# Kernel tuning notes

Measured on AMD Instinct MI355X. Metric: run time of the kernel, lower is better.

## Reference

```python
import jax, jax.numpy as jnp
import numpy as np

N_OBJ = 1280
N_REL = 32768
HID = 512
POOL = 4096
N_OBJ_CLS = 151
N_REL_CLS = 51


def setup_inputs() -> dict:
    key = jax.random.key(0)
    ks = jax.random.split(key, 11)
    s = lambda d: 1.0 / np.sqrt(d)
    return {
        "edge_ctx": jax.random.normal(ks[0], (N_OBJ, HID), jnp.float32),
        "union_features": jax.random.normal(ks[1], (N_REL, POOL), jnp.float32),
        "w_post_emb": jax.random.normal(ks[2], (HID, 2 * HID), jnp.float32) * (10.0 * s(HID)),
        "b_post_emb": jax.random.normal(ks[3], (2 * HID,), jnp.float32) * 0.01,
        "w_post_cat": jax.random.normal(ks[4], (2 * HID, POOL), jnp.float32) * s(2 * HID),
        "b_post_cat": jnp.zeros((POOL,), jnp.float32),
        "w_ctx": jax.random.normal(ks[5], (POOL, N_REL_CLS), jnp.float32) * s(POOL),
        "b_ctx": jnp.zeros((N_REL_CLS,), jnp.float32),
        "freq_table": jax.random.normal(ks[6], (N_OBJ_CLS * N_OBJ_CLS, N_REL_CLS), jnp.float32),
        "obj_preds": jax.random.randint(ks[7], (N_OBJ,), 0, N_OBJ_CLS, jnp.int64),
        "pair_idx": jax.random.randint(ks[8], (N_REL, 2), 0, N_OBJ, jnp.int64),
    }


def reference(edge_ctx, union_features, w_post_emb, b_post_emb, w_post_cat,
              b_post_cat, w_ctx, b_ctx, freq_table, obj_preds, pair_idx):
    # edge_rep = relu(post_emb(edge_ctx)) viewed as [N_obj, 2, HID]
    edge_rep = jax.nn.relu(edge_ctx @ w_post_emb + b_post_emb)  # [N_obj, 2*HID]
    head_rep = edge_rep[:, :HID]   # [N_obj, HID]
    tail_rep = edge_rep[:, HID:]   # [N_obj, HID]
    # gather per-pair head/tail reps (pair_idx already globalized across images)
    prod_rep = jnp.concatenate(
        (head_rep[pair_idx[:, 0]], tail_rep[pair_idx[:, 1]]), axis=-1)  # [N_rel, 2*HID]
    prod_rep = prod_rep @ w_post_cat + b_post_cat                      # [N_rel, POOL]
    # elementwise fuse with visual union features, then compress to rel logits
    ctx_dists = (prod_rep * union_features) @ w_ctx + b_ctx            # [N_rel, 51]
    # frequency-bias embedding lookup on (subj_class, obj_class) pair
    pair_pred = jnp.stack((obj_preds[pair_idx[:, 0]], obj_preds[pair_idx[:, 1]]), axis=1)
    frq_dists = freq_table[pair_pred[:, 0] * N_OBJ_CLS + pair_pred[:, 1]]
    rel_dists = ctx_dists + frq_dists
    return rel_dists
```

## Files before the change

### kernel.cpp

```cpp
#include <hip/hip_runtime.h>

typedef __attribute__((ext_vector_type(8))) short bf16x8;
typedef __attribute__((ext_vector_type(4))) float f32x4;

__device__ __forceinline__ float bf2f(short s) {
    union { unsigned int i; float f; } v;
    v.i = ((unsigned int)(unsigned short)s) << 16;
    return v.f;
}
__device__ __forceinline__ short f2bf(float f) {
    unsigned int x = __float_as_uint(f);
    unsigned int r = (x + 0x7fffu + ((x >> 16) & 1u)) >> 16;
    return (short)r;
}

__global__ __launch_bounds__(256) void transpose_cvt(
    const float* __restrict__ in, short* __restrict__ out,
    int R, int C, int Cout)
{
    __shared__ short tile[64][65];
    const int r0 = blockIdx.x << 6;
    const int c0 = blockIdx.y << 6;
    const int t = threadIdx.x;
#pragma unroll
    for (int i = 0; i < 16; ++i) {
        int idx = t + (i << 8);
        int rr = idx >> 6, cc = idx & 63;
        int c = c0 + cc;
        tile[rr][cc] = (c < C) ? f2bf(in[(size_t)(r0 + rr) * C + c]) : (short)0;
    }
    __syncthreads();
#pragma unroll
    for (int i = 0; i < 16; ++i) {
        int idx = t + (i << 8);
        int cc = idx >> 6, rr = idx & 63;
        out[(size_t)(c0 + cc) * R + r0 + rr] = tile[rr][cc];
    }
}

template<int A_F32>
__global__ __launch_bounds__(256) void gemm_bt(
    const void* __restrict__ Ap, int lda,
    const short* __restrict__ Bt, int ldb,
    const float* __restrict__ bias,
    short* __restrict__ C, int ldc,
    int K, int relu)
{
    __shared__ short As[64][72];
    __shared__ short Bs[64][72];
    const int t = threadIdx.x;
    const int wave = t >> 6;
    const int lane = t & 63;
    const int m0 = blockIdx.x << 6;
    const int n0 = blockIdx.y << 6;

    const int rr = t >> 2;
    const int kc = (t & 3) << 4;
    const float* apf = (const float*)Ap + (size_t)(m0 + rr) * lda + kc;
    const short* aps = (const short*)Ap + (size_t)(m0 + rr) * lda + kc;
    const short* bp  = Bt + (size_t)(n0 + rr) * ldb + kc;

    f32x4 acc[4];
#pragma unroll
    for (int i = 0; i < 4; ++i) acc[i] = (f32x4){0.f, 0.f, 0.f, 0.f};

    const int ml = lane & 15;
    const int kq = (lane >> 4) << 3;

    for (int k0 = 0; k0 < K; k0 += 64) {
        bf16x8 a0, a1;
        if (A_F32) {
            float4 x0 = *(const float4*)(apf + k0);
            float4 x1 = *(const float4*)(apf + k0 + 4);
            float4 x2 = *(const float4*)(apf + k0 + 8);
            float4 x3 = *(const float4*)(apf + k0 + 12);
            a0[0] = f2bf(x0.x); a0[1] = f2bf(x0.y); a0[2] = f2bf(x0.z); a0[3] = f2bf(x0.w);
            a0[4] = f2bf(x1.x); a0[5] = f2bf(x1.y); a0[6] = f2bf(x1.z); a0[7] = f2bf(x1.w);
            a1[0] = f2bf(x2.x); a1[1] = f2bf(x2.y); a1[2] = f2bf(x2.z); a1[3] = f2bf(x2.w);
            a1[4] = f2bf(x3.x); a1[5] = f2bf(x3.y); a1[6] = f2bf(x3.z); a1[7] = f2bf(x3.w);
        } else {
            a0 = *(const bf16x8*)(aps + k0);
            a1 = *(const bf16x8*)(aps + k0 + 8);
        }
        bf16x8 b0 = *(const bf16x8*)(bp + k0);
        bf16x8 b1 = *(const bf16x8*)(bp + k0 + 8);
        __syncthreads();
        *(bf16x8*)&As[rr][kc]     = a0;
        *(bf16x8*)&As[rr][kc + 8] = a1;
        *(bf16x8*)&Bs[rr][kc]     = b0;
        *(bf16x8*)&Bs[rr][kc + 8] = b1;
        __syncthreads();
#pragma unroll
        for (int ks = 0; ks < 64; ks += 32) {
            bf16x8 af = *(const bf16x8*)&As[(wave << 4) + ml][ks + kq];
#pragma unroll
            for (int nb = 0; nb < 4; ++nb) {
                bf16x8 bfr = *(const bf16x8*)&Bs[(nb << 4) + ml][ks + kq];
                acc[nb] = __builtin_amdgcn_mfma_f32_16x16x32_bf16(af, bfr, acc[nb], 0, 0, 0);
            }
        }
    }

    const int ql = lane >> 4;
#pragma unroll
    for (int reg = 0; reg < 4; ++reg) {
        int r = m0 + (wave << 4) + (ql << 2) + reg;
#pragma unroll
        for (int nb = 0; nb < 4; ++nb) {
            int c = n0 + (nb << 4) + ml;
            float v = acc[nb][reg];
            if (bias) v += bias[c];
            if (relu) v = fmaxf(v, 0.f);
            C[(size_t)r * ldc + c] = f2bf(v);
        }
    }
}

__global__ __launch_bounds__(256) void fused_rel(
    const float* __restrict__ U,
    const short* __restrict__ Hm,
    const short* __restrict__ Tm,
    const short* __restrict__ Wt,
    const float* __restrict__ bcat,
    const float* __restrict__ bctx,
    const float* __restrict__ freq,
    const int* __restrict__ obj_preds,
    const int* __restrict__ pair_idx,
    float* __restrict__ out)
{
    __shared__ short As[64][72];
    __shared__ short Bs[64][72];
    const int t = threadIdx.x;
    const int wave = t >> 6;
    const int lane = t & 63;
    const int r0 = blockIdx.x << 6;

    const int rr = t >> 2;
    const int kc = (t & 3) << 4;

    const int r = r0 + rr;
    const int p0 = pair_idx[2 * r];
    const int p1 = pair_idx[2 * r + 1];

    const float* up = U + (size_t)r * 4096 + kc;
    const short* hp = Hm + (size_t)p0 * 4096 + kc;
    const short* tp = Tm + (size_t)p1 * 4096 + kc;
    const short* wp = Wt + (size_t)rr * 4096 + kc;
    const float* bp = bcat + kc;

    f32x4 acc[4];
#pragma unroll
    for (int i = 0; i < 4; ++i) acc[i] = (f32x4){0.f, 0.f, 0.f, 0.f};

    const int ml = lane & 15;
    const int kq = (lane >> 4) << 3;

    for (int k0 = 0; k0 < 4096; k0 += 64) {
        float4 u0 = *(const float4*)(up + k0);
        float4 u1 = *(const float4*)(up + k0 + 4);
        float4 u2 = *(const float4*)(up + k0 + 8);
        float4 u3 = *(const float4*)(up + k0 + 12);
        float4 c0 = *(const float4*)(bp + k0);
        float4 c1 = *(const float4*)(bp + k0 + 4);
        float4 c2 = *(const float4*)(bp + k0 + 8);
        float4 c3 = *(const float4*)(bp + k0 + 12);
        bf16x8 h0 = *(const bf16x8*)(hp + k0);
        bf16x8 h1 = *(const bf16x8*)(hp + k0 + 8);
        bf16x8 t0 = *(const bf16x8*)(tp + k0);
        bf16x8 t1 = *(const bf16x8*)(tp + k0 + 8);
        bf16x8 w0 = *(const bf16x8*)(wp + k0);
        bf16x8 w1 = *(const bf16x8*)(wp + k0 + 8);

        float uu[16] = {u0.x,u0.y,u0.z,u0.w, u1.x,u1.y,u1.z,u1.w,
                        u2.x,u2.y,u2.z,u2.w, u3.x,u3.y,u3.z,u3.w};
        float bb[16] = {c0.x,c0.y,c0.z,c0.w, c1.x,c1.y,c1.z,c1.w,
                        c2.x,c2.y,c2.z,c2.w, c3.x,c3.y,c3.z,c3.w};

        bf16x8 a0, a1;
#pragma unroll
        for (int j = 0; j < 8; ++j) {
            a0[j] = f2bf((bf2f(h0[j]) + bf2f(t0[j]) + bb[j])     * uu[j]);
            a1[j] = f2bf((bf2f(h1[j]) + bf2f(t1[j]) + bb[8 + j]) * uu[8 + j]);
        }
        __syncthreads();
        *(bf16x8*)&As[rr][kc]     = a0;
        *(bf16x8*)&As[rr][kc + 8] = a1;
        *(bf16x8*)&Bs[rr][kc]     = w0;
        *(bf16x8*)&Bs[rr][kc + 8] = w1;
        __syncthreads();
#pragma unroll
        for (int ks = 0; ks < 64; ks += 32) {
            bf16x8 af = *(const bf16x8*)&As[(wave << 4) + ml][ks + kq];
#pragma unroll
            for (int nb = 0; nb < 4; ++nb) {
                bf16x8 bfr = *(const bf16x8*)&Bs[(nb << 4) + ml][ks + kq];
                acc[nb] = __builtin_amdgcn_mfma_f32_16x16x32_bf16(af, bfr, acc[nb], 0, 0, 0);
            }
        }
    }

    const int ql = lane >> 4;
#pragma unroll
    for (int reg = 0; reg < 4; ++reg) {
        int rm = r0 + (wave << 4) + (ql << 2) + reg;
        int q0 = pair_idx[2 * rm];
        int q1 = pair_idx[2 * rm + 1];
        int code = obj_preds[q0] * 151 + obj_preds[q1];
        const float* fr = freq + (size_t)code * 51;
#pragma unroll
        for (int nb = 0; nb < 4; ++nb) {
            int c = (nb << 4) + ml;
            if (c < 51) {
                out[(size_t)rm * 51 + c] = acc[nb][reg] + bctx[c] + fr[c];
            }
        }
    }
}

extern "C" void kernel_launch(void* const* d_in, const int* in_sizes, int n_in,
                              void* d_out, int out_size, void* d_ws, size_t ws_size,
                              hipStream_t stream)
{
    (void)in_sizes; (void)n_in; (void)out_size; (void)ws_size;

    const float* edge_ctx = (const float*)d_in[0];
    const float* unionf   = (const float*)d_in[1];
    const float* w_emb    = (const float*)d_in[2];
    const float* b_emb    = (const float*)d_in[3];
    const float* w_cat    = (const float*)d_in[4];
    const float* b_cat    = (const float*)d_in[5];
    const float* w_ctx    = (const float*)d_in[6];
    const float* b_ctx    = (const float*)d_in[7];
    const float* freq     = (const float*)d_in[8];
    const int*   obj_pred = (const int*)d_in[9];
    const int*   pair_idx = (const int*)d_in[10];
    float* out = (float*)d_out;

    char* ws = (char*)d_ws;
    short* WembT    = (short*)(ws);
    short* WcatT    = (short*)(ws + (1ull  << 20));
    short* Wt       = (short*)(ws + (9ull  << 20));
    short* edge_rep = (short*)(ws + (10ull << 20));
    short* Hbuf     = (short*)(ws + (13ull << 20));
    short* Tbuf     = (short*)(ws + (23ull << 20));

    transpose_cvt<<<dim3(8, 16),  256, 0, stream>>>(w_emb, WembT, 512, 1024, 1024);
    transpose_cvt<<<dim3(16, 64), 256, 0, stream>>>(w_cat, WcatT, 1024, 4096, 4096);
    transpose_cvt<<<dim3(64, 1),  256, 0, stream>>>(w_ctx, Wt, 4096, 51, 64);

    gemm_bt<1><<<dim3(20, 16), 256, 0, stream>>>(edge_ctx, 512, WembT, 512,
                                                 b_emb, edge_rep, 1024, 512, 1);

    gemm_bt<0><<<dim3(20, 64), 256, 0, stream>>>(edge_rep, 1024, WcatT, 1024,
                                                 nullptr, Hbuf, 4096, 512, 0);
    gemm_bt<0><<<dim3(20, 64), 256, 0, stream>>>(edge_rep + 512, 1024, WcatT + 512, 1024,
                                                 nullptr, Tbuf, 4096, 512, 0);

    fused_rel<<<dim3(512), 256, 0, stream>>>(unionf, Hbuf, Tbuf, Wt, b_cat, b_ctx,
                                             freq, obj_pred, pair_idx, out);
}
```

Baseline: 831.9 us.

## Load MFMA fragments directly from global memory, dropping LDS staging and barriers

Both the GEMM kernel and the fused relation kernel stop staging A and B tiles through shared memory with two barriers per K step. Each lane now loads its MFMA operand fragments straight from global memory, with a 32-wide K step unrolled twice. The post_cat bias is moved into the head GEMM epilogue, so the fused kernel no longer loads it. The trade-off is that B rows are no longer shared through LDS: every wave loads the same weight fragments redundantly and the global access pattern is less coalesced.

Measured after the change: 964.5 us. 1.16x slower.

```diff
diff --git a/kernel.cpp b/kernel.cpp
--- a/kernel.cpp
+++ b/kernel.cpp
@@ -46,59 +46,45 @@
     short* __restrict__ C, int ldc,
     int K, int relu)
 {
-    __shared__ short As[64][72];
-    __shared__ short Bs[64][72];
     const int t = threadIdx.x;
     const int wave = t >> 6;
     const int lane = t & 63;
+    const int ml = lane & 15;
+    const int kq = (lane >> 4) << 3;
     const int m0 = blockIdx.x << 6;
     const int n0 = blockIdx.y << 6;
 
-    const int rr = t >> 2;
-    const int kc = (t & 3) << 4;
-    const float* apf = (const float*)Ap + (size_t)(m0 + rr) * lda + kc;
-    const short* aps = (const short*)Ap + (size_t)(m0 + rr) * lda + kc;
-    const short* bp  = Bt + (size_t)(n0 + rr) * ldb + kc;
+    const int arow = m0 + (wave << 4) + ml;
+    const float* apf = (const float*)Ap + (size_t)arow * lda + kq;
+    const short* aps = (const short*)Ap + (size_t)arow * lda + kq;
+    const short* bp0 = Bt + (size_t)(n0 + ml) * ldb + kq;
+    const short* bp1 = bp0 + (size_t)16 * ldb;
+    const short* bp2 = bp0 + (size_t)32 * ldb;
+    const short* bp3 = bp0 + (size_t)48 * ldb;
 
     f32x4 acc[4];
 #pragma unroll
     for (int i = 0; i < 4; ++i) acc[i] = (f32x4){0.f, 0.f, 0.f, 0.f};
 
-    const int ml = lane & 15;
-    const int kq = (lane >> 4) << 3;
-
-    for (int k0 = 0; k0 < K; k0 += 64) {
-        bf16x8 a0, a1;
+#pragma unroll 2
+    for (int k0 = 0; k0 < K; k0 += 32) {
+        bf16x8 a;
         if (A_F32) {
             float4 x0 = *(const float4*)(apf + k0);
             float4 x1 = *(const float4*)(apf + k0 + 4);
-            float4 x2 = *(const float4*)(apf + k0 + 8);
-            float4 x3 = *(const float4*)(apf + k0 + 12);
-            a0[0] = f2bf(x0.x); a0[1] = f2bf(x0.y); a0[2] = f2bf(x0.z); a0[3] = f2bf(x0.w);
-            a0[4] = f2bf(x1.x); a0[5] = f2bf(x1.y); a0[6] = f2bf(x1.z); a0[7] = f2bf(x1.w);
-            a1[0] = f2bf(x2.x); a1[1] = f2bf(x2.y); a1[2] = f2bf(x2.z); a1[3] = f2bf(x2.w);
-            a1[4] = f2bf(x3.x); a1[5] = f2bf(x3.y); a1[6] = f2bf(x3.z); a1[7] = f2bf(x3.w);
+            a[0] = f2bf(x0.x); a[1] = f2bf(x0.y); a[2] = f2bf(x0.z); a[3] = f2bf(x0.w);
+            a[4] = f2bf(x1.x); a[5] = f2bf(x1.y); a[6] = f2bf(x1.z); a[7] = f2bf(x1.w);
         } else {
-            a0 = *(const bf16x8*)(aps + k0);
-            a1 = *(const bf16x8*)(aps + k0 + 8);
+            a = *(const bf16x8*)(aps + k0);
         }
-        bf16x8 b0 = *(const bf16x8*)(bp + k0);
-        bf16x8 b1 = *(const bf16x8*)(bp + k0 + 8);
-        __syncthreads();
-        *(bf16x8*)&As[rr][kc]     = a0;
-        *(bf16x8*)&As[rr][kc + 8] = a1;
-        *(bf16x8*)&Bs[rr][kc]     = b0;
-        *(bf16x8*)&Bs[rr][kc + 8] = b1;
-        __syncthreads();
-#pragma unroll
-        for (int ks = 0; ks < 64; ks += 32) {
-            bf16x8 af = *(const bf16x8*)&As[(wave << 4) + ml][ks + kq];
-#pragma unroll
-            for (int nb = 0; nb < 4; ++nb) {
-                bf16x8 bfr = *(const bf16x8*)&Bs[(nb << 4) + ml][ks + kq];
-                acc[nb] = __builtin_amdgcn_mfma_f32_16x16x32_bf16(af, bfr, acc[nb], 0, 0, 0);
-            }
-        }
+        bf16x8 b0 = *(const bf16x8*)(bp0 + k0);
+        bf16x8 b1 = *(const bf16x8*)(bp1 + k0);
+        bf16x8 b2 = *(const bf16x8*)(bp2 + k0);
+        bf16x8 b3 = *(const bf16x8*)(bp3 + k0);
+        acc[0] = __builtin_amdgcn_mfma_f32_16x16x32_bf16(a, b0, acc[0], 0, 0, 0);
+        acc[1] = __builtin_amdgcn_mfma_f32_16x16x32_bf16(a, b1, acc[1], 0, 0, 0);
+        acc[2] = __builtin_amdgcn_mfma_f32_16x16x32_bf16(a, b2, acc[2], 0, 0, 0);
+        acc[3] = __builtin_amdgcn_mfma_f32_16x16x32_bf16(a, b3, acc[3], 0, 0, 0);
     }
 
     const int ql = lane >> 4;
@@ -121,97 +107,71 @@
     const short* __restrict__ Hm,
     const short* __restrict__ Tm,
     const short* __restrict__ Wt,
-    const float* __restrict__ bcat,
     const float* __restrict__ bctx,
     const float* __restrict__ freq,
     const int* __restrict__ obj_preds,
     const int* __restrict__ pair_idx,
     float* __restrict__ out)
 {
-    __shared__ short As[64][72];
-    __shared__ short Bs[64][72];
     const int t = threadIdx.x;
     const int wave = t >> 6;
     const int lane = t & 63;
-    const int r0 = blockIdx.x << 6;
-
-    const int rr = t >> 2;
-    const int kc = (t & 3) << 4;
-
-    const int r = r0 + rr;
-    const int p0 = pair_idx[2 * r];
-    const int p1 = pair_idx[2 * r + 1];
-
-    const float* up = U + (size_t)r * 4096 + kc;
-    const short* hp = Hm + (size_t)p0 * 4096 + kc;
-    const short* tp = Tm + (size_t)p1 * 4096 + kc;
-    const short* wp = Wt + (size_t)rr * 4096 + kc;
-    const float* bp = bcat + kc;
-
-    f32x4 acc[4];
-#pragma unroll
-    for (int i = 0; i < 4; ++i) acc[i] = (f32x4){0.f, 0.f, 0.f, 0.f};
-
     const int ml = lane & 15;
     const int kq = (lane >> 4) << 3;
-
-    for (int k0 = 0; k0 < 4096; k0 += 64) {
+    const int r0 = blockIdx.x << 6;
+    const int rm = r0 + (wave << 4) + ml;
+
+    const int p0 = pair_idx[2 * rm];
+    const int p1 = pair_idx[2 * rm + 1];
+
+    const float* up  = U  + (size_t)rm * 4096 + kq;
+    const short* hp  = Hm + (size_t)p0 * 4096 + kq;
+    const short* tp  = Tm + (size_t)p1 * 4096 + kq;
+    const short* wp0 = Wt + (size_t)ml * 4096 + kq;
+    const short* wp1 = wp0 + 16 * 4096;
+    const short* wp2 = wp0 + 32 * 4096;
+    const short* wp3 = wp0 + 48 * 4096;
+
+    f32x4 acc[4];
+#pragma unroll
+    for (int i = 0; i < 4; ++i) acc[i] = (f32x4){0.f, 0.f, 0.f, 0.f};
+
+#pragma unroll 2
+    for (int k0 = 0; k0 < 4096; k0 += 32) {
         float4 u0 = *(const float4*)(up + k0);
         float4 u1 = *(const float4*)(up + k0 + 4);
-        float4 u2 = *(const float4*)(up + k0 + 8);
-        float4 u3 = *(const float4*)(up + k0 + 12);
-        float4 c0 = *(const float4*)(bp + k0);
-        float4 c1 = *(const float4*)(bp + k0 + 4);
-        float4 c2 = *(const float4*)(bp + k0 + 8);
-        float4 c3 = *(const float4*)(bp + k0 + 12);
-        bf16x8 h0 = *(const bf16x8*)(hp + k0);
-        bf16x8 h1 = *(const bf16x8*)(hp + k0 + 8);
-        bf16x8 t0 = *(const bf16x8*)(tp + k0);
-        bf16x8 t1 = *(const bf16x8*)(tp + k0 + 8);
-        bf16x8 w0 = *(const bf16x8*)(wp + k0);
-        bf16x8 w1 = *(const bf16x8*)(wp + k0 + 8);
-
-        float uu[16] = {u0.x,u0.y,u0.z,u0.w, u1.x,u1.y,u1.z,u1.w,
-                        u2.x,u2.y,u2.z,u2.w, u3.x,u3.y,u3.z,u3.w};
-        float bb[16] = {c0.x,c0.y,c0.z,c0.w, c1.x,c1.y,c1.z,c1.w,
-                        c2.x,c2.y,c2.z,c2.w, c3.x,c3.y,c3.z,c3.w};
-
-        bf16x8 a0, a1;
-#pragma unroll
-        for (int j = 0; j < 8; ++j) {
-            a0[j] = f2bf((bf2f(h0[j]) + bf2f(t0[j]) + bb[j])     * uu[j]);
-            a1[j] = f2bf((bf2f(h1[j]) + bf2f(t1[j]) + bb[8 + j]) * uu[8 + j]);
-        }
-        __syncthreads();
-        *(bf16x8*)&As[rr][kc]     = a0;
-        *(bf16x8*)&As[rr][kc + 8] = a1;
-        *(bf16x8*)&Bs[rr][kc]     = w0;
-        *(bf16x8*)&Bs[rr][kc + 8] = w1;
-        __syncthreads();
-#pragma unroll
-        for (int ks = 0; ks < 64; ks += 32) {
-            bf16x8 af = *(const bf16x8*)&As[(wave << 4) + ml][ks + kq];
-#pragma unroll
-            for (int nb = 0; nb < 4; ++nb) {
-                bf16x8 bfr = *(const bf16x8*)&Bs[(nb << 4) + ml][ks + kq];
-                acc[nb] = __builtin_amdgcn_mfma_f32_16x16x32_bf16(af, bfr, acc[nb], 0, 0, 0);
-            }
-        }
+        bf16x8 h  = *(const bf16x8*)(hp + k0);
+        bf16x8 tv = *(const bf16x8*)(tp + k0);
+        bf16x8 b0 = *(const bf16x8*)(wp0 + k0);
+        bf16x8 b1 = *(const bf16x8*)(wp1 + k0);
+        bf16x8 b2 = *(const bf16x8*)(wp2 + k0);
+        bf16x8 b3 = *(const bf16x8*)(wp3 + k0);
+
+        float uu[8] = {u0.x, u0.y, u0.z, u0.w, u1.x, u1.y, u1.z, u1.w};
+        bf16x8 a;
+#pragma unroll
+        for (int j = 0; j < 8; ++j)
+            a[j] = f2bf((bf2f(h[j]) + bf2f(tv[j])) * uu[j]);
+
+        acc[0] = __builtin_amdgcn_mfma_f32_16x16x32_bf16(a, b0, acc[0], 0, 0, 0);
+        acc[1] = __builtin_amdgcn_mfma_f32_16x16x32_bf16(a, b1, acc[1], 0, 0, 0);
+        acc[2] = __builtin_amdgcn_mfma_f32_16x16x32_bf16(a, b2, acc[2], 0, 0, 0);
+        acc[3] = __builtin_amdgcn_mfma_f32_16x16x32_bf16(a, b3, acc[3], 0, 0, 0);
     }
 
     const int ql = lane >> 4;
 #pragma unroll
     for (int reg = 0; reg < 4; ++reg) {
-        int rm = r0 + (wave << 4) + (ql << 2) + reg;
-        int q0 = pair_idx[2 * rm];
-        int q1 = pair_idx[2 * rm + 1];
+        int rr = r0 + (wave << 4) + (ql << 2) + reg;
+        int q0 = pair_idx[2 * rr];
+        int q1 = pair_idx[2 * rr + 1];
         int code = obj_preds[q0] * 151 + obj_preds[q1];
         const float* fr = freq + (size_t)code * 51;
 #pragma unroll
         for (int nb = 0; nb < 4; ++nb) {
             int c = (nb << 4) + ml;
             if (c < 51) {
-                out[(size_t)rm * 51 + c] = acc[nb][reg] + bctx[c] + fr[c];
+                out[(size_t)rr * 51 + c] = acc[nb][reg] + bctx[c] + fr[c];
             }
         }
     }
@@ -252,10 +212,10 @@
                                                  b_emb, edge_rep, 1024, 512, 1);
 
     gemm_bt<0><<<dim3(20, 64), 256, 0, stream>>>(edge_rep, 1024, WcatT, 1024,
-                                                 nullptr, Hbuf, 4096, 512, 0);
+                                                 b_cat, Hbuf, 4096, 512, 0);
     gemm_bt<0><<<dim3(20, 64), 256, 0, stream>>>(edge_rep + 512, 1024, WcatT + 512, 1024,
                                                  nullptr, Tbuf, 4096, 512, 0);
 
-    fused_rel<<<dim3(512), 256, 0, stream>>>(unionf, Hbuf, Tbuf, Wt, b_cat, b_ctx,
+    fused_rel<<<dim3(512), 256, 0, stream>>>(unionf, Hbuf, Tbuf, Wt, b_ctx,
                                              freq, obj_pred, pair_idx, out);
 }
```

## Double-buffer LDS with XOR swizzle and fold cat bias into head GEMM

Applied to the files above, without the earlier changes.

Both the generic GEMM and the fused relation kernel now double-buffer their shared-memory tiles. Each iteration issues the global loads for the next K step before the MFMA loop, which leaves one barrier per step instead of two. The padded LDS layout is replaced by an XOR swizzle on 8-element groups to avoid bank conflicts without padding. The post_cat bias is added in the Hbuf GEMM epilogue rather than per element in the fused kernel, which cuts one bias load stream there but rounds the bias into the bf16 head buffer.

Measured after the change: 830.5 us. No clear change (-0.2%).

```diff
diff --git a/kernel.cpp b/kernel.cpp
--- a/kernel.cpp
+++ b/kernel.cpp
@@ -46,56 +46,80 @@
     short* __restrict__ C, int ldc,
     int K, int relu)
 {
-    __shared__ short As[64][72];
-    __shared__ short Bs[64][72];
+    __shared__ short As[2][64][64];
+    __shared__ short Bs[2][64][64];
     const int t = threadIdx.x;
     const int wave = t >> 6;
     const int lane = t & 63;
+    const int ml = lane & 15;
+    const int kq = (lane >> 4) << 3;
     const int m0 = blockIdx.x << 6;
     const int n0 = blockIdx.y << 6;
 
     const int rr = t >> 2;
     const int kc = (t & 3) << 4;
+    const int wg0 = (((kc >> 3) ^ (rr & 7)) << 3);
+    const int wg1 = ((((kc >> 3) + 1) ^ (rr & 7)) << 3);
+
     const float* apf = (const float*)Ap + (size_t)(m0 + rr) * lda + kc;
     const short* aps = (const short*)Ap + (size_t)(m0 + rr) * lda + kc;
     const short* bp  = Bt + (size_t)(n0 + rr) * ldb + kc;
 
+    const int x7 = ml & 7;
+    const int arow = (wave << 4) + ml;
+
     f32x4 acc[4];
 #pragma unroll
     for (int i = 0; i < 4; ++i) acc[i] = (f32x4){0.f, 0.f, 0.f, 0.f};
 
-    const int ml = lane & 15;
-    const int kq = (lane >> 4) << 3;
-
-    for (int k0 = 0; k0 < K; k0 += 64) {
+    float4 x0, x1, x2, x3;
+    bf16x8 a0s, a1s, b0s, b1s;
+    if (A_F32) {
+        x0 = *(const float4*)(apf);     x1 = *(const float4*)(apf + 4);
+        x2 = *(const float4*)(apf + 8); x3 = *(const float4*)(apf + 12);
+    } else {
+        a0s = *(const bf16x8*)(aps);
+        a1s = *(const bf16x8*)(aps + 8);
+    }
+    b0s = *(const bf16x8*)(bp);
+    b1s = *(const bf16x8*)(bp + 8);
+
+    const int NS = K >> 6;
+    for (int s = 0; s < NS; ++s) {
+        const int cur = s & 1;
         bf16x8 a0, a1;
         if (A_F32) {
-            float4 x0 = *(const float4*)(apf + k0);
-            float4 x1 = *(const float4*)(apf + k0 + 4);
-            float4 x2 = *(const float4*)(apf + k0 + 8);
-            float4 x3 = *(const float4*)(apf + k0 + 12);
             a0[0] = f2bf(x0.x); a0[1] = f2bf(x0.y); a0[2] = f2bf(x0.z); a0[3] = f2bf(x0.w);
             a0[4] = f2bf(x1.x); a0[5] = f2bf(x1.y); a0[6] = f2bf(x1.z); a0[7] = f2bf(x1.w);
             a1[0] = f2bf(x2.x); a1[1] = f2bf(x2.y); a1[2] = f2bf(x2.z); a1[3] = f2bf(x2.w);
             a1[4] = f2bf(x3.x); a1[5] = f2bf(x3.y); a1[6] = f2bf(x3.z); a1[7] = f2bf(x3.w);
         } else {
-            a0 = *(const bf16x8*)(aps + k0);
-            a1 = *(const bf16x8*)(aps + k0 + 8);
-        }
-        bf16x8 b0 = *(const bf16x8*)(bp + k0);
-        bf16x8 b1 = *(const bf16x8*)(bp + k0 + 8);
+            a0 = a0s; a1 = a1s;
+        }
+        *(bf16x8*)&As[cur][rr][wg0] = a0;
+        *(bf16x8*)&As[cur][rr][wg1] = a1;
+        *(bf16x8*)&Bs[cur][rr][wg0] = b0s;
+        *(bf16x8*)&Bs[cur][rr][wg1] = b1s;
         __syncthreads();
-        *(bf16x8*)&As[rr][kc]     = a0;
-        *(bf16x8*)&As[rr][kc + 8] = a1;
-        *(bf16x8*)&Bs[rr][kc]     = b0;
-        *(bf16x8*)&Bs[rr][kc + 8] = b1;
-        __syncthreads();
+        if (s + 1 < NS) {
+            const int k0 = (s + 1) << 6;
+            if (A_F32) {
+                x0 = *(const float4*)(apf + k0);     x1 = *(const float4*)(apf + k0 + 4);
+                x2 = *(const float4*)(apf + k0 + 8); x3 = *(const float4*)(apf + k0 + 12);
+            } else {
+                a0s = *(const bf16x8*)(aps + k0);
+                a1s = *(const bf16x8*)(aps + k0 + 8);
+            }
+            b0s = *(const bf16x8*)(bp + k0);
+            b1s = *(const bf16x8*)(bp + k0 + 8);
+        }
 #pragma unroll
         for (int ks = 0; ks < 64; ks += 32) {
-            bf16x8 af = *(const bf16x8*)&As[(wave << 4) + ml][ks + kq];
+            const int gb = (ks + kq) >> 3;
+            bf16x8 af = *(const bf16x8*)&As[cur][arow][((gb ^ x7) << 3)];
 #pragma unroll
             for (int nb = 0; nb < 4; ++nb) {
-                bf16x8 bfr = *(const bf16x8*)&Bs[(nb << 4) + ml][ks + kq];
+                bf16x8 bfr = *(const bf16x8*)&Bs[cur][(nb << 4) + ml][((gb ^ x7) << 3)];
                 acc[nb] = __builtin_amdgcn_mfma_f32_16x16x32_bf16(af, bfr, acc[nb], 0, 0, 0);
             }
         }
@@ -121,22 +145,25 @@
     const short* __restrict__ Hm,
     const short* __restrict__ Tm,
     const short* __restrict__ Wt,
-    const float* __restrict__ bcat,
     const float* __restrict__ bctx,
     const float* __restrict__ freq,
     const int* __restrict__ obj_preds,
     const int* __restrict__ pair_idx,
     float* __restrict__ out)
 {
-    __shared__ short As[64][72];
-    __shared__ short Bs[64][72];
+    __shared__ short As[2][64][64];
+    __shared__ short Bs[2][64][64];
     const int t = threadIdx.x;
     const int wave = t >> 6;
     const int lane = t & 63;
+    const int ml = lane & 15;
+    const int kq = (lane >> 4) << 3;
     const int r0 = blockIdx.x << 6;
 
     const int rr = t >> 2;
     const int kc = (t & 3) << 4;
+    const int wg0 = (((kc >> 3) ^ (rr & 7)) << 3);
+    const int wg1 = ((((kc >> 3) + 1) ^ (rr & 7)) << 3);
 
     const int r = r0 + rr;
     const int p0 = pair_idx[2 * r];
@@ -146,58 +173,61 @@
     const short* hp = Hm + (size_t)p0 * 4096 + kc;
     const short* tp = Tm + (size_t)p1 * 4096 + kc;
     const short* wp = Wt + (size_t)rr * 4096 + kc;
-    const float* bp = bcat + kc;
+
+    const int x7 = ml & 7;
+    const int arow = (wave << 4) + ml;
 
     f32x4 acc[4];
 #pragma unroll
     for (int i = 0; i < 4; ++i) acc[i] = (f32x4){0.f, 0.f, 0.f, 0.f};
 
-    const int ml = lane & 15;
-    const int kq = (lane >> 4) << 3;
-
-    for (int k0 = 0; k0 < 4096; k0 += 64) {
-        float4 u0 = *(const float4*)(up + k0);
-        float4 u1 = *(const float4*)(up + k0 + 4);
-        float4 u2 = *(const float4*)(up + k0 + 8);
-        float4 u3 = *(const float4*)(up + k0 + 12);
-        float4 c0 = *(const float4*)(bp + k0);
-        float4 c1 = *(const float4*)(bp + k0 + 4);
-        float4 c2 = *(const float4*)(bp + k0 + 8);
-        float4 c3 = *(const float4*)(bp + k0 + 12);
-        bf16x8 h0 = *(const bf16x8*)(hp + k0);
-        bf16x8 h1 = *(const bf16x8*)(hp + k0 + 8);
-        bf16x8 t0 = *(const bf16x8*)(tp + k0);
-        bf16x8 t1 = *(const bf16x8*)(tp + k0 + 8);
-        bf16x8 w0 = *(const bf16x8*)(wp + k0);
-        bf16x8 w1 = *(const bf16x8*)(wp + k0 + 8);
-
-        float uu[16] = {u0.x,u0.y,u0.z,u0.w, u1.x,u1.y,u1.z,u1.w,
-                        u2.x,u2.y,u2.z,u2.w, u3.x,u3.y,u3.z,u3.w};
-        float bb[16] = {c0.x,c0.y,c0.z,c0.w, c1.x,c1.y,c1.z,c1.w,
-                        c2.x,c2.y,c2.z,c2.w, c3.x,c3.y,c3.z,c3.w};
-
+    float4 u0, u1, u2, u3;
+    bf16x8 h0, h1, t0, t1, w0, w1;
+#define LOADG(K0)                                            \
+    u0 = *(const float4*)(up + (K0));                        \
+    u1 = *(const float4*)(up + (K0) + 4);                    \
+    u2 = *(const float4*)(up + (K0) + 8);                    \
+    u3 = *(const float4*)(up + (K0) + 12);                   \
+    h0 = *(const bf16x8*)(hp + (K0));                        \
+    h1 = *(const bf16x8*)(hp + (K0) + 8);                    \
+    t0 = *(const bf16x8*)(tp + (K0));                        \
+    t1 = *(const bf16x8*)(tp + (K0) + 8);                    \
+    w0 = *(const bf16x8*)(wp + (K0));                        \
+    w1 = *(const bf16x8*)(wp + (K0) + 8)
+
+    LOADG(0);
+
+    for (int s = 0; s < 64; ++s) {
+        const int cur = s & 1;
+        float uu[16] = {u0.x, u0.y, u0.z, u0.w, u1.x, u1.y, u1.z, u1.w,
+                        u2.x, u2.y, u2.z, u2.w, u3.x, u3.y, u3.z, u3.w};
         bf16x8 a0, a1;
 #pragma unroll
         for (int j = 0; j < 8; ++j) {
-            a0[j] = f2bf((bf2f(h0[j]) + bf2f(t0[j]) + bb[j])     * uu[j]);
-            a1[j] = f2bf((bf2f(h1[j]) + bf2f(t1[j]) + bb[8 + j]) * uu[8 + j]);
-        }
+            a0[j] = f2bf((bf2f(h0[j]) + bf2f(t0[j])) * uu[j]);
+            a1[j] = f2bf((bf2f(h1[j]) + bf2f(t1[j])) * uu[8 + j]);
+        }
+        *(bf16x8*)&As[cur][rr][wg0] = a0;
+        *(bf16x8*)&As[cur][rr][wg1] = a1;
+        *(bf16x8*)&Bs[cur][rr][wg0] = w0;
+        *(bf16x8*)&Bs[cur][rr][wg1] = w1;
         __syncthreads();
-        *(bf16x8*)&As[rr][kc]     = a0;
-        *(bf16x8*)&As[rr][kc + 8] = a1;
-        *(bf16x8*)&Bs[rr][kc]     = w0;
-        *(bf16x8*)&Bs[rr][kc + 8] = w1;
-        __syncthreads();
+        if (s + 1 < 64) {
+            const int k0 = (s + 1) << 6;
+            LOADG(k0);
+        }
 #pragma unroll
         for (int ks = 0; ks < 64; ks += 32) {
-            bf16x8 af = *(const bf16x8*)&As[(wave << 4) + ml][ks + kq];
+            const int gb = (ks + kq) >> 3;
+            bf16x8 af = *(const bf16x8*)&As[cur][arow][((gb ^ x7) << 3)];
 #pragma unroll
             for (int nb = 0; nb < 4; ++nb) {
-                bf16x8 bfr = *(const bf16x8*)&Bs[(nb << 4) + ml][ks + kq];
+                bf16x8 bfr = *(const bf16x8*)&Bs[cur][(nb << 4) + ml][((gb ^ x7) << 3)];
                 acc[nb] = __builtin_amdgcn_mfma_f32_16x16x32_bf16(af, bfr, acc[nb], 0, 0, 0);
             }
         }
     }
+#undef LOADG
 
     const int ql = lane >> 4;
 #pragma unroll
@@ -252,10 +282,10 @@
                                                  b_emb, edge_rep, 1024, 512, 1);
 
     gemm_bt<0><<<dim3(20, 64), 256, 0, stream>>>(edge_rep, 1024, WcatT, 1024,
-                                                 nullptr, Hbuf, 4096, 512, 0);
+                                                 b_cat, Hbuf, 4096, 512, 0);
     gemm_bt<0><<<dim3(20, 64), 256, 0, stream>>>(edge_rep + 512, 1024, WcatT + 512, 1024,
                                                  nullptr, Tbuf, 4096, 512, 0);
 
-    fused_rel<<<dim3(512), 256, 0, stream>>>(unionf, Hbuf, Tbuf, Wt, b_cat, b_ctx,
+    fused_rel<<<dim3(512), 256, 0, stream>>>(unionf, Hbuf, Tbuf, Wt, b_ctx,
                                              freq, obj_pred, pair_idx, out);
 }
```
